# Kernel tuning notes

Measured on AMD Instinct MI355X. Metric: run time of the kernel, lower is better.

Reference implementation:

```python
import jax, jax.numpy as jnp
import numpy as np

B, S, D, H = 8, 1024, 2048, 16
DH = D // H  # 128


def setup_inputs() -> dict:
    key = jax.random.key(0)
    ks = jax.random.split(key, 6)
    sc = 1.0 / np.sqrt(D)
    return {
        "q": jax.random.normal(ks[0], (B, S, D), jnp.float32),
        "k": jax.random.normal(ks[1], (B, S, D), jnp.float32),
        "v": jax.random.normal(ks[2], (B, S, D), jnp.float32),
        "Wq": jax.random.normal(ks[3], (D, D), jnp.float32) * sc,
        "Wk": jax.random.normal(ks[4], (D, D), jnp.float32) * sc,
        "Wv": jax.random.normal(ks[5], (D, D), jnp.float32) * sc,
    }


def reference(q, k, v, Wq, Wk, Wv):
    # Linear projections (no bias), then split feature dim into H heads of DH.
    qh = (q @ Wq).reshape(B, S, H, DH)
    kh = (k @ Wk).reshape(B, S, H, DH)
    vh = (v @ Wv).reshape(B, S, H, DH)
    # scores: [B, H, Sq, Sk], scaled by sqrt(d_head)
    scores = jnp.einsum("bqhd,bkhd->bhqk", qh, kh) / jnp.sqrt(
        jnp.asarray(DH, qh.dtype)
    )
    probs = jax.nn.softmax(scores, axis=-1)
    out = jnp.einsum("bhqk,bkhd->bqhd", probs, vh).reshape(B, S, D)
    return out.astype(jnp.float32)
```

## Files before the change

### kernel.cpp

```cpp
#include <hip/hip_runtime.h>
#include <hip/hip_bf16.h>
#include <math.h>

#define BB 8
#define SS 1024
#define DD 2048
#define HH 16
#define DHD 128

typedef float  v4f  __attribute__((ext_vector_type(4)));
typedef short  v4s  __attribute__((ext_vector_type(4)));
typedef short  v8s  __attribute__((ext_vector_type(8)));
typedef __bf16 v8bf __attribute__((ext_vector_type(8)));

#define GLOBAL_AS __attribute__((address_space(1)))
#define LDS_AS    __attribute__((address_space(3)))

__device__ __forceinline__ v8bf ldsv8(const unsigned short* p) {
    return __builtin_bit_cast(v8bf, *(const v8s*)p);
}

__device__ __forceinline__ short bfb(float x) {
    return __builtin_bit_cast(short, (__bf16)x);
}

__device__ __forceinline__ unsigned short f2b(float f) {
    union { float f; unsigned int u; } x; x.f = f;
    unsigned int r = x.u + 0x7fffu + ((x.u >> 16) & 1u);
    return (unsigned short)(r >> 16);
}

__global__ __launch_bounds__(256) void wtrans_all(const float* __restrict__ W0,
                                                  const float* __restrict__ W1,
                                                  const float* __restrict__ W2,
                                                  unsigned short* __restrict__ T0,
                                                  unsigned short* __restrict__ T1,
                                                  unsigned short* __restrict__ T2) {
    const float* W = blockIdx.z == 0 ? W0 : (blockIdx.z == 1 ? W1 : W2);
    unsigned short* WT = blockIdx.z == 0 ? T0 : (blockIdx.z == 1 ? T1 : T2);
    __shared__ float t[64][65];
    int nb = blockIdx.x * 64;
    int kb = blockIdx.y * 64;
    int tr = threadIdx.x >> 4;
    int tc = (threadIdx.x & 15) * 4;
#pragma unroll
    for (int i = 0; i < 4; i++) {
        int k = kb + tr + i * 16;
        v4f v = *(const v4f*)(W + (size_t)k * DD + nb + tc);
        t[tr + i * 16][tc + 0] = v[0];
        t[tr + i * 16][tc + 1] = v[1];
        t[tr + i * 16][tc + 2] = v[2];
        t[tr + i * 16][tc + 3] = v[3];
    }
    __syncthreads();
#pragma unroll
    for (int i = 0; i < 4; i++) {
        int n = nb + tr + i * 16;
        v4s o;
#pragma unroll
        for (int j = 0; j < 4; j++) o[j] = bfb(t[tc + j][tr + i * 16]);
        *(v4s*)(WT + (size_t)n * DD + kb + tc) = o;
    }
}


#define STAGE_B(bb, gg, tt) do {                                              \
    __builtin_amdgcn_global_load_lds(                                         \
        (const GLOBAL_AS void*)(pB0 + (size_t)(gg) * 32 * DD + (size_t)(tt) * 64), \
        (LDS_AS void*)(&sB[(bb) * 16384 + ldsB0 + (gg) * 2048]), 16, 0, 0);   \
    __builtin_amdgcn_global_load_lds(                                         \
        (const GLOBAL_AS void*)(pB1 + (size_t)(gg) * 32 * DD + (size_t)(tt) * 64), \
        (LDS_AS void*)(&sB[(bb) * 16384 + ldsB1 + (gg) * 2048]), 16, 0, 0);   \
} while (0)

#define ALOAD(tt) do {                                                        \
    ar[0][0][0] = *(const v4f*)(qA0 + (size_t)(tt) * 64);                     \
    ar[0][0][1] = *(const v4f*)(qA0 + (size_t)(tt) * 64 + 4);                 \
    ar[0][1][0] = *(const v4f*)(qA1 + (size_t)(tt) * 64);                     \
    ar[0][1][1] = *(const v4f*)(qA1 + (size_t)(tt) * 64 + 4);                 \
    ar[1][0][0] = *(const v4f*)(qA0 + (size_t)64 * DD + (size_t)(tt) * 64);   \
    ar[1][0][1] = *(const v4f*)(qA0 + (size_t)64 * DD + (size_t)(tt) * 64 + 4); \
    ar[1][1][0] = *(const v4f*)(qA1 + (size_t)64 * DD + (size_t)(tt) * 64);   \
    ar[1][1][1] = *(const v4f*)(qA1 + (size_t)64 * DD + (size_t)(tt) * 64 + 4); \
} while (0)

#define PACK8(dst, va, vb) do {                                               \
    v8s _o;                                                                   \
    _o[0] = bfb((va)[0]); _o[1] = bfb((va)[1]);                               \
    _o[2] = bfb((va)[2]); _o[3] = bfb((va)[3]);                               \
    _o[4] = bfb((vb)[0]); _o[5] = bfb((vb)[1]);                               \
    _o[6] = bfb((vb)[2]); _o[7] = bfb((vb)[3]);                               \
    *(v8s*)(dst) = _o;                                                        \
} while (0)

#define AWRITE(bb, gg) do {                                                   \
    PACK8(&sA[(bb) * 16384 + (raA0 + (gg) * 64 + l3) * 64 + l7 * 8],          \
          ar[gg][0][0], ar[gg][0][1]);                                        \
    PACK8(&sA[(bb) * 16384 + (raA1 + (gg) * 64 + l3) * 64 + l7 * 8],          \
          ar[gg][1][0], ar[gg][1][1]);                                        \
} while (0)

#define LDA(mh) do {                                                          \
    _Pragma("unroll")                                                         \
    for (int i = 0; i < 4; i++) {                                             \
        af[i][0] = ldsv8(sAb + aRow + (mh) * 4096 + i * 1024 + c0);           \
        af[i][1] = ldsv8(sAb + aRow + (mh) * 4096 + i * 1024 + c1);           \
    }                                                                         \
} while (0)

#define LDB(nh) do {                                                          \
    _Pragma("unroll")                                                         \
    for (int j = 0; j < 2; j++) {                                             \
        bf2[j][0] = ldsv8(sBb + bRow + (nh) * 2048 + j * 1024 + c0);          \
        bf2[j][1] = ldsv8(sBb + bRow + (nh) * 2048 + j * 1024 + c1);          \
    }                                                                         \
} while (0)

#define MMA(mh, nh) do {                                                      \
    _Pragma("unroll")                                                         \
    for (int i = 0; i < 4; i++) {                                             \
        _Pragma("unroll")                                                     \
        for (int j = 0; j < 2; j++)                                           \
            acc[(mh) * 4 + i][(nh) * 2 + j] =                                 \
                __builtin_amdgcn_mfma_f32_16x16x32_bf16(                      \
                    af[i][0], bf2[j][0], acc[(mh) * 4 + i][(nh) * 2 + j], 0, 0, 0); \
    }                                                                         \
    _Pragma("unroll")                                                         \
    for (int i = 0; i < 4; i++) {                                             \
        _Pragma("unroll")                                                     \
        for (int j = 0; j < 2; j++)                                           \
            acc[(mh) * 4 + i][(nh) * 2 + j] =                                 \
                __builtin_amdgcn_mfma_f32_16x16x32_bf16(                      \
                    af[i][1], bf2[j][1], acc[(mh) * 4 + i][(nh) * 2 + j], 0, 0, 0); \
    }                                                                         \
} while (0)

#define QSCALE 0.12753139626246937f

__global__ __launch_bounds__(512, 2) void gemm_all(
        const float* __restrict__ Aq, const float* __restrict__ Ak,
        const float* __restrict__ Av,
        const unsigned short* __restrict__ Bq, const unsigned short* __restrict__ Bk,
        const unsigned short* __restrict__ Bv,
        unsigned short* __restrict__ Cq, unsigned short* __restrict__ Ck,
        unsigned short* __restrict__ Cv) {
    __shared__ __align__(16) unsigned short sA[2 * 16384];
    __shared__ __align__(16) unsigned short sB[2 * 16384];

    const int proj = blockIdx.y;
    const float* A; const unsigned short* BT; unsigned short* C;
    float scale; int vmode;
    if (proj == 0)      { A = Aq; BT = Bq; C = Cq; scale = QSCALE; vmode = 0; }
    else if (proj == 1) { A = Ak; BT = Bk; C = Ck; scale = 1.f;    vmode = 0; }
    else                { A = Av; BT = Bv; C = Cv; scale = 1.f;    vmode = 1; }

    const int tid  = threadIdx.x;
    const int lane = tid & 63;
    const int w    = tid >> 6;
    const int qcol = lane & 15;
    const int quad = lane >> 4;
    const int l3   = lane >> 3;
    const int l7   = lane & 7;

    const int bid = blockIdx.x;
    const int bm  = ((bid & 7) * 4 + ((bid >> 3) & 3)) * 256;
    const int bn  = (bid >> 5) * 256;

    const int wm = (w >> 2) * 128;
    const int wn = (w & 3) * 64;

    const int gchunk = (l7 ^ l3) * 8;
    const int iA0 = w * 2, iA1 = w * 2 + 1;
    const int raA0 = (iA0 >> 3) * 128 + (iA0 & 7) * 8;
    const int raA1 = (iA1 >> 3) * 128 + (iA1 & 7) * 8;
    const int rbB0 = (iA0 >> 2) * 64 + (iA0 & 3) * 8;
    const int rbB1 = (iA1 >> 2) * 64 + (iA1 & 3) * 8;
    const float* qA0 = A + (size_t)(bm + raA0 + l3) * DD + gchunk;
    const float* qA1 = A + (size_t)(bm + raA1 + l3) * DD + gchunk;
    const unsigned short* pB0 = BT + (size_t)(bn + rbB0 + l3) * DD + gchunk;
    const unsigned short* pB1 = BT + (size_t)(bn + rbB1 + l3) * DD + gchunk;
    const int ldsB0 = rbB0 * 64, ldsB1 = rbB1 * 64;

    const int c0   = ((quad ^ l7) & 7) * 8;
    const int c1   = c0 ^ 32;
    const int aRow = (wm + qcol) * 64;
    const int bRow = (wn + qcol) * 64;

    v4f acc[8][4];
#pragma unroll
    for (int i = 0; i < 8; i++)
#pragma unroll
        for (int j = 0; j < 4; j++) acc[i][j] = (v4f){0.f, 0.f, 0.f, 0.f};

    v8bf af[4][2];
    v8bf bf2[2][2];
    v4f  ar[2][2][2];

    const int nt = DD >> 6;

    STAGE_B(0, 0, 0);
    STAGE_B(0, 1, 0);
    ALOAD(0);
    AWRITE(0, 0);
    AWRITE(0, 1);
    asm volatile("s_waitcnt vmcnt(0) lgkmcnt(0)");
    __builtin_amdgcn_s_barrier();

    for (int t = 0; t < nt - 1; ++t) {
        const int buf = t & 1, nbuf = buf ^ 1;
        const unsigned short* sAb = &sA[buf * 16384];
        const unsigned short* sBb = &sB[buf * 16384];

        STAGE_B(nbuf, 0, t + 1);
        STAGE_B(nbuf, 1, t + 1);
        ALOAD(t + 1);
        LDA(0); LDB(0);
        MMA(0, 0);
        LDB(1);
        MMA(0, 1);
        __builtin_amdgcn_sched_barrier(0);
        LDA(1);
        MMA(1, 1);
        LDB(0);
        MMA(1, 0);
        AWRITE(nbuf, 0);
        AWRITE(nbuf, 1);
        asm volatile("s_waitcnt vmcnt(0) lgkmcnt(0)");
        __builtin_amdgcn_sched_barrier(0);
        __builtin_amdgcn_s_barrier();
    }

    {
        const int buf = (nt - 1) & 1;
        const unsigned short* sAb = &sA[buf * 16384];
        const unsigned short* sBb = &sB[buf * 16384];
        LDA(0); LDB(0); MMA(0, 0);
        LDB(1);         MMA(0, 1);
        LDA(1);         MMA(1, 1);
        LDB(0);         MMA(1, 0);
    }

    if (vmode == 0) {
#pragma unroll
        for (int mi = 0; mi < 8; mi++)
#pragma unroll
            for (int nj = 0; nj < 4; nj++)
#pragma unroll
                for (int r = 0; r < 4; r++) {
                    int row = bm + wm + mi * 16 + quad * 4 + r;
                    int col = bn + wn + nj * 16 + qcol;
                    C[(size_t)row * DD + col] = (unsigned short)bfb(acc[mi][nj][r] * scale);
                }
    } else {
#pragma unroll
        for (int mi = 0; mi < 8; mi++)
#pragma unroll
            for (int nj = 0; nj < 4; nj++)
#pragma unroll
                for (int r = 0; r < 4; r++) {
                    int row = bm + wm + mi * 16 + quad * 4 + r;
                    int col = bn + wn + nj * 16 + qcol;
                    size_t idx = ((size_t)(row >> 10) * 2048 + col) * 1024 + (row & 1023);
                    C[idx] = (unsigned short)bfb(acc[mi][nj][r] * scale);
                }
    }
}

__global__ __launch_bounds__(256, 4) void attn_kernel(const unsigned short* __restrict__ qh,
                                                      const unsigned short* __restrict__ kh,
                                                      const unsigned short* __restrict__ vt,
                                                      float* __restrict__ out) {
    __shared__ __align__(16) unsigned short sK[64 * 128];
    __shared__ __align__(16) unsigned short sV[128 * 64];
    __shared__ __align__(16) unsigned short sP[4 * 16 * 64];

    int lane = threadIdx.x & 63, w = threadIdx.x >> 6;
    int b = blockIdx.z, h = blockIdx.y;
    int q0 = blockIdx.x * 64 + w * 16;
    int qcol = lane & 15, quad = lane >> 4;

    const unsigned short* qp = qh + (size_t)(b * SS + q0 + qcol) * DD + h * DHD;
    v8bf bq[4];
#pragma unroll
    for (int kk = 0; kk < 4; kk++)
        bq[kk] = __builtin_bit_cast(v8bf, *(const v8s*)(qp + kk * 32 + quad * 8));

    int ko[4];
#pragma unroll
    for (int j = 0; j < 4; j++) {
        int key = w * 16 + j * 4 + (lane >> 4);
        ko[j] = key * DD + (((lane & 15) ^ (key & 15)) * 8);
    }
    int vo0 = (w * 32 + (lane >> 3)) * SS + (((lane & 7) ^ (lane >> 3)) * 8);

    const unsigned short* kcur = kh + (size_t)b * SS * DD + h * DHD;
    const unsigned short* vcur = vt + (size_t)(b * HH + h) * DHD * SS;
    unsigned short* kl0 = &sK[(w * 16) * 128];
    unsigned short* vl0 = &sV[(w * 32) * 64];
    unsigned short* sPw = &sP[w * 1024];

    int pw[4], pr[2];
#pragma unroll
    for (int kf = 0; kf < 4; kf++)
        pw[kf] = qcol * 64 + (((kf * 2 + (quad >> 1)) ^ (qcol & 7)) * 8) + (quad & 1) * 4;
#pragma unroll
    for (int ks = 0; ks < 2; ks++)
        pr[ks] = qcol * 64 + (((ks * 4 + quad) ^ (qcol & 7)) * 8);

    float m_i = -1e30f, l_i = 0.f;
    v4f acc[8];
#pragma unroll
    for (int c = 0; c < 8; c++) acc[c] = (v4f){0.f, 0.f, 0.f, 0.f};

    for (int kb = 0; kb < SS; kb += 64) {
        __syncthreads();
#pragma unroll
        for (int j = 0; j < 4; j++)
            __builtin_amdgcn_global_load_lds((const GLOBAL_AS void*)(kcur + ko[j]),
                                             (LDS_AS void*)(kl0 + j * 4 * 128), 16, 0, 0);
#pragma unroll
        for (int j = 0; j < 4; j++)
            __builtin_amdgcn_global_load_lds((const GLOBAL_AS void*)(vcur + vo0 + j * 8 * SS),
                                             (LDS_AS void*)(vl0 + j * 8 * 64), 16, 0, 0);
        kcur += (size_t)64 * DD;
        vcur += 64;
        __syncthreads();

        v4f s[4];
#pragma unroll
        for (int kf = 0; kf < 4; kf++) {
            s[kf] = (v4f){0.f, 0.f, 0.f, 0.f};
#pragma unroll
            for (int kk = 0; kk < 4; kk++) {
                v8bf ak = __builtin_bit_cast(v8bf,
                    *(const v8s*)&sK[(kf * 16 + qcol) * 128 + (((kk * 4 + quad) ^ qcol) * 8)]);
                s[kf] = __builtin_amdgcn_mfma_f32_16x16x32_bf16(ak, bq[kk], s[kf], 0, 0, 0);
            }
        }

        float mx = -1e30f;
#pragma unroll
        for (int kf = 0; kf < 4; kf++)
#pragma unroll
            for (int r = 0; r < 4; r++) mx = fmaxf(mx, s[kf][r]);
        mx = fmaxf(mx, __shfl_xor(mx, 16));
        mx = fmaxf(mx, __shfl_xor(mx, 32));
        float m_new = fmaxf(m_i, mx);
        float rs = 0.f;
        v4s p[4];
#pragma unroll
        for (int kf = 0; kf < 4; kf++)
#pragma unroll
            for (int r = 0; r < 4; r++) {
                float pf = exp2f(s[kf][r] - m_new);
                rs += pf;
                p[kf][r] = (short)f2b(pf);
            }
        rs += __shfl_xor(rs, 16);
        rs += __shfl_xor(rs, 32);
        if (__any(mx > m_i)) {
            float alpha = exp2f(m_i - m_new);
            l_i *= alpha;
#pragma unroll
            for (int c = 0; c < 8; c++) {
                acc[c][0] *= alpha; acc[c][1] *= alpha;
                acc[c][2] *= alpha; acc[c][3] *= alpha;
            }
        }
        l_i += rs;
        m_i = m_new;

#pragma unroll
        for (int kf = 0; kf < 4; kf++)
            *(v4s*)&sPw[pw[kf]] = p[kf];

#pragma unroll
        for (int ks = 0; ks < 2; ks++) {
            v8bf pb = ldsv8(&sPw[pr[ks]]);
#pragma unroll
            for (int c = 0; c < 8; c++) {
                v8bf av = ldsv8(&sV[(c * 16 + qcol) * 64 + (((ks * 4 + quad) ^ (qcol & 7)) * 8)]);
                acc[c] = __builtin_amdgcn_mfma_f32_16x16x32_bf16(av, pb, acc[c], 0, 0, 0);
            }
        }
    }

    float rl = 1.0f / l_i;
    float* op = out + (size_t)(b * SS + q0 + qcol) * DD + h * DHD;
#pragma unroll
    for (int c = 0; c < 8; c++)
#pragma unroll
        for (int r = 0; r < 4; r++)
            op[c * 16 + quad * 4 + r] = acc[c][r] * rl;
}

extern "C" void kernel_launch(void* const* d_in, const int* in_sizes, int n_in,
                              void* d_out, int out_size, void* d_ws, size_t ws_size,
                              hipStream_t stream) {
    const float* q  = (const float*)d_in[0];
    const float* k  = (const float*)d_in[1];
    const float* v  = (const float*)d_in[2];
    const float* Wq = (const float*)d_in[3];
    const float* Wk = (const float*)d_in[4];
    const float* Wv = (const float*)d_in[5];
    char* ws = (char*)d_ws;
    unsigned short* wq  = (unsigned short*)(ws);
    unsigned short* wk  = (unsigned short*)(ws + (size_t)8  * 1024 * 1024);
    unsigned short* wv  = (unsigned short*)(ws + (size_t)16 * 1024 * 1024);
    unsigned short* qhb = (unsigned short*)(ws + (size_t)24 * 1024 * 1024);
    unsigned short* khb = (unsigned short*)(ws + (size_t)56 * 1024 * 1024);
    unsigned short* vtb = (unsigned short*)(ws + (size_t)88 * 1024 * 1024);
    float* out = (float*)d_out;

    wtrans_all<<<dim3(32, 32, 3), dim3(256), 0, stream>>>(Wq, Wk, Wv, wq, wk, wv);
    gemm_all<<<dim3(256, 3), dim3(512), 0, stream>>>(q, k, v, wq, wk, wv, qhb, khb, vtb);
    attn_kernel<<<dim3(SS / 64, HH, BB), dim3(256), 0, stream>>>(qhb, khb, vtb, out);
}
```

Before: 556.6 us.

## Prefetch fp32 A tiles two stages ahead and preload all B fragments

Restructures the projection GEMM main loop so the fp32 A global loads are issued two iterations ahead in registers. They are converted and written to LDS one iteration later, with partial vmcnt waits in place of full drains, and a peeled second-to-last iteration handles the tail. All four B fragment pairs are now loaded from LDS once per tile, which removes the repeated B reloads. The MFMA blocks are wrapped in s_setprio so the matrix issue gets priority. This raises register pressure from the extra in-flight A tile and the larger B fragment array, which could lower occupancy under launch_bounds(512,2).

```diff
diff --git a/kernel.cpp b/kernel.cpp
--- a/kernel.cpp
+++ b/kernel.cpp
@@ -108,22 +108,24 @@
     }                                                                         \
 } while (0)
 
-#define LDB(nh) do {                                                          \
+#define LDBALL() do {                                                         \
     _Pragma("unroll")                                                         \
-    for (int j = 0; j < 2; j++) {                                             \
-        bf2[j][0] = ldsv8(sBb + bRow + (nh) * 2048 + j * 1024 + c0);          \
-        bf2[j][1] = ldsv8(sBb + bRow + (nh) * 2048 + j * 1024 + c1);          \
+    for (int n = 0; n < 4; n++) {                                             \
+        bfall[n][0] = ldsv8(sBb + bRow + n * 1024 + c0);                      \
+        bfall[n][1] = ldsv8(sBb + bRow + n * 1024 + c1);                      \
     }                                                                         \
 } while (0)
 
 #define MMA(mh, nh) do {                                                      \
+    __builtin_amdgcn_s_setprio(1);                                            \
     _Pragma("unroll")                                                         \
     for (int i = 0; i < 4; i++) {                                             \
         _Pragma("unroll")                                                     \
         for (int j = 0; j < 2; j++)                                           \
             acc[(mh) * 4 + i][(nh) * 2 + j] =                                 \
                 __builtin_amdgcn_mfma_f32_16x16x32_bf16(                      \
-                    af[i][0], bf2[j][0], acc[(mh) * 4 + i][(nh) * 2 + j], 0, 0, 0); \
+                    af[i][0], bfall[(nh) * 2 + j][0],                         \
+                    acc[(mh) * 4 + i][(nh) * 2 + j], 0, 0, 0);                \
     }                                                                         \
     _Pragma("unroll")                                                         \
     for (int i = 0; i < 4; i++) {                                             \
@@ -131,8 +133,10 @@
         for (int j = 0; j < 2; j++)                                           \
             acc[(mh) * 4 + i][(nh) * 2 + j] =                                 \
                 __builtin_amdgcn_mfma_f32_16x16x32_bf16(                      \
-                    af[i][1], bf2[j][1], acc[(mh) * 4 + i][(nh) * 2 + j], 0, 0, 0); \
+                    af[i][1], bfall[(nh) * 2 + j][1],                         \
+                    acc[(mh) * 4 + i][(nh) * 2 + j], 0, 0, 0);                \
     }                                                                         \
+    __builtin_amdgcn_s_setprio(0);                                            \
 } while (0)
 
 #define QSCALE 0.12753139626246937f
@@ -193,38 +197,67 @@
         for (int j = 0; j < 4; j++) acc[i][j] = (v4f){0.f, 0.f, 0.f, 0.f};
 
     v8bf af[4][2];
-    v8bf bf2[2][2];
+    v8bf bfall[4][2];
     v4f  ar[2][2][2];
 
     const int nt = DD >> 6;
 
+    ALOAD(0);
     STAGE_B(0, 0, 0);
     STAGE_B(0, 1, 0);
-    ALOAD(0);
+    asm volatile("s_waitcnt vmcnt(4)");
     AWRITE(0, 0);
     AWRITE(0, 1);
-    asm volatile("s_waitcnt vmcnt(0) lgkmcnt(0)");
+    ALOAD(1);
+    __builtin_amdgcn_sched_barrier(0);
+    asm volatile("s_waitcnt vmcnt(8) lgkmcnt(0)");
+    __builtin_amdgcn_sched_barrier(0);
     __builtin_amdgcn_s_barrier();
 
-    for (int t = 0; t < nt - 1; ++t) {
+    for (int t = 0; t < nt - 2; ++t) {
         const int buf = t & 1, nbuf = buf ^ 1;
         const unsigned short* sAb = &sA[buf * 16384];
         const unsigned short* sBb = &sB[buf * 16384];
 
         STAGE_B(nbuf, 0, t + 1);
         STAGE_B(nbuf, 1, t + 1);
-        ALOAD(t + 1);
-        LDA(0); LDB(0);
+        asm volatile("s_waitcnt vmcnt(4)");
+        AWRITE(nbuf, 0);
+        AWRITE(nbuf, 1);
+        ALOAD(t + 2);
+        __builtin_amdgcn_sched_barrier(0);
+
+        LDA(0); LDBALL();
         MMA(0, 0);
-        LDB(1);
         MMA(0, 1);
-        __builtin_amdgcn_sched_barrier(0);
         LDA(1);
         MMA(1, 1);
-        LDB(0);
         MMA(1, 0);
+
+        asm volatile("s_waitcnt vmcnt(8) lgkmcnt(0)");
+        __builtin_amdgcn_sched_barrier(0);
+        __builtin_amdgcn_s_barrier();
+    }
+
+    {
+        const int t = nt - 2;
+        const int buf = t & 1, nbuf = buf ^ 1;
+        const unsigned short* sAb = &sA[buf * 16384];
+        const unsigned short* sBb = &sB[buf * 16384];
+
+        STAGE_B(nbuf, 0, t + 1);
+        STAGE_B(nbuf, 1, t + 1);
+        asm volatile("s_waitcnt vmcnt(4)");
         AWRITE(nbuf, 0);
         AWRITE(nbuf, 1);
+
+        LDA(0); LDBALL();
+        MMA(0, 0);
+        MMA(0, 1);
+        LDA(1);
+        MMA(1, 1);
+        MMA(1, 0);
+
         asm volatile("s_waitcnt vmcnt(0) lgkmcnt(0)");
         __builtin_amdgcn_sched_barrier(0);
         __builtin_amdgcn_s_barrier();
@@ -234,10 +267,12 @@
         const int buf = (nt - 1) & 1;
         const unsigned short* sAb = &sA[buf * 16384];
         const unsigned short* sBb = &sB[buf * 16384];
-        LDA(0); LDB(0); MMA(0, 0);
-        LDB(1);         MMA(0, 1);
-        LDA(1);         MMA(1, 1);
-        LDB(0);         MMA(1, 0);
+        LDA(0); LDBALL();
+        MMA(0, 0);
+        MMA(0, 1);
+        LDA(1);
+        MMA(1, 1);
+        MMA(1, 0);
     }
 
     if (vmode == 0) {
```

Measured after the change: 569.0 us. 1.02x slower.
